# Kernel optimization log

Measured on AMD Instinct MI355X. Metric: run time of the kernel, lower is better.

## Reference

```python
import jax, jax.numpy as jnp
import numpy as np

N, T, D_FEAT, H = 8192, 60, 6, 64
NEG_SLOPE = 0.01  # torch LeakyReLU default


def setup_inputs() -> dict:
    key = jax.random.key(0)
    ks = jax.random.split(key, 20)
    s = lambda k, shape, fan: jax.random.normal(k, shape, jnp.float32) * (1.0 / np.sqrt(fan))
    inp = {
        'x': jax.random.normal(ks[0], (N, T, D_FEAT), jnp.float32),
        # LSTM layer 0 (input D_FEAT) and layer 1 (input H); gate order i,f,g,o
        'Wih0': s(ks[1], (4 * H, D_FEAT), H), 'Whh0': s(ks[2], (4 * H, H), H),
        'bih0': s(ks[3], (4 * H,), H), 'bhh0': s(ks[4], (4 * H,), H),
        'Wih1': s(ks[5], (4 * H, H), H), 'Whh1': s(ks[6], (4 * H, H), H),
        'bih1': s(ks[7], (4 * H,), H), 'bhh1': s(ks[8], (4 * H,), H),
        # GAT layer: transformation Linear(H,H) and attention vector a [2H,1] (randn in torch)
        'Wt': s(ks[9], (H, H), H), 'bt': s(ks[10], (H,), H),
        'a': jax.random.normal(ks[11], (2 * H, 1), jnp.float32),
        # fc and fc_out
        'Wfc': s(ks[12], (H, H), H), 'bfc': s(ks[13], (H,), H),
        'Wout': s(ks[14], (1, H), H), 'bout': s(ks[15], (1,), H),
    }
    return inp


def _lstm_layer(x, Wih, Whh, bih, bhh):
    # x: [N, T, Din] -> outputs [N, T, H]
    xg = jnp.einsum('ntd,gd->ntg', x, Wih) + bih + bhh  # precompute input gates

    def step(carry, xt):
        h, c = carry
        gates = xt + h @ Whh.T  # [N, 4H]
        i, f, g, o = jnp.split(gates, 4, axis=-1)
        c = jax.nn.sigmoid(f) * c + jax.nn.sigmoid(i) * jnp.tanh(g)
        h = jax.nn.sigmoid(o) * jnp.tanh(c)
        return (h, c), h

    n = x.shape[0]
    h0 = jnp.zeros((n, Whh.shape[1]), x.dtype)
    (_, _), hs = jax.lax.scan(step, (h0, h0), jnp.swapaxes(xg, 0, 1))
    return jnp.swapaxes(hs, 0, 1)


def _gat_layer(x, Wt, bt, a):
    # att[i,j] = leaky_relu(a1 . Wx_j + a2 . Wx_i); softmax over j; out = att @ x
    h = x @ Wt.T + bt                    # [N, H]
    hdim = h.shape[1]
    s1 = (h @ a[:hdim]).squeeze(-1)      # a1 . Wx_j  -> column term
    s2 = (h @ a[hdim:]).squeeze(-1)      # a2 . Wx_i  -> row term
    scores = jax.nn.leaky_relu(s2[:, None] + s1[None, :], NEG_SLOPE)  # [N, N]
    att = jax.nn.softmax(scores, axis=1)
    return att @ x


def reference(x, Wih0, Whh0, bih0, bhh0, Wih1, Whh1, bih1, bhh1,
              Wt, bt, a, Wfc, bfc, Wout, bout):
    out = _lstm_layer(x, Wih0, Whh0, bih0, bhh0)
    out = _lstm_layer(out, Wih1, Whh1, bih1, bhh1)
    last = out[:, -1, :]                 # [N, H]
    hidden = _gat_layer(last, Wt, bt, a) + last  # num_layers_gat = 1
    hidden = jax.nn.leaky_relu(hidden @ Wfc.T + bfc, NEG_SLOPE)
    return (hidden @ Wout.T + bout).squeeze(-1)  # [N]
```

## Files before the change

### kernel.cpp

```cpp
#include <hip/hip_runtime.h>

#define NN 8192
#define TT 60
#define DF 6
#define HH 64
#define GG 256
#define RS 132
#define CH 32
#define NB 256

typedef _Float16 half8 __attribute__((ext_vector_type(8)));
typedef float f32x4 __attribute__((ext_vector_type(4)));
#define MFMA16(a, b, c) __builtin_amdgcn_mfma_f32_16x16x32_f16((a), (b), (c), 0, 0, 0)

#define LOG2E 1.44269504f

__device__ __forceinline__ float lrelu_(float x) { return x > 0.0f ? x : 0.01f * x; }

__device__ __forceinline__ float lstm_act2s(float gi, float gf, float gg, float go,
                                            float& c)
{
    const float ei = __builtin_amdgcn_exp2f(gi);
    const float ef = __builtin_amdgcn_exp2f(gf);
    const float eg = __builtin_amdgcn_exp2f(fminf(gg, 63.f));
    const float sf = __builtin_amdgcn_rcpf(1.f + ef);
    const float tg_si = (1.f - eg) * __builtin_amdgcn_rcpf((1.f + ei) * (1.f + eg));
    c = __builtin_fmaf(sf, c, tg_si);
    const float eo = __builtin_amdgcn_exp2f(go);
    const float ec = __builtin_amdgcn_exp2f(fminf(c * (-2.f * LOG2E), 63.f));
    return (1.f - ec) * __builtin_amdgcn_rcpf((1.f + eo) * (1.f + ec));
}

__device__ __forceinline__ half8 ldw8s(const float* __restrict__ p, float s) {
    const float4* q = (const float4*)p;
    float4 u = q[0], v = q[1];
    half8 r;
    r[0]=(_Float16)(u.x*s); r[1]=(_Float16)(u.y*s); r[2]=(_Float16)(u.z*s); r[3]=(_Float16)(u.w*s);
    r[4]=(_Float16)(v.x*s); r[5]=(_Float16)(v.y*s); r[6]=(_Float16)(v.z*s); r[7]=(_Float16)(v.w*s);
    return r;
}

#define SXW (TT * 8 + 8)

__global__ __launch_bounds__(512, 4)
void lstm_fused_kernel(const float* __restrict__ x,
                       const float* __restrict__ Wih0, const float* __restrict__ Whh0,
                       const float* __restrict__ bih0, const float* __restrict__ bhh0,
                       const float* __restrict__ Wih1, const float* __restrict__ Whh1,
                       const float* __restrict__ bih1, const float* __restrict__ bhh1,
                       const float* __restrict__ Wt, const float* __restrict__ bt,
                       const float* __restrict__ av,
                       float* __restrict__ last_out,
                       float* __restrict__ s1g, float* __restrict__ s2g)
{
    __shared__ _Float16 sxp[16][SXW];
    __shared__ _Float16 h0buf[2][16][72];
    __shared__ _Float16 h1buf[2][16][72];
    __shared__ _Float16 zero16[8];
    __shared__ float sv1[HH], sv2[HH], sc12[2];

    const int tid  = threadIdx.x;
    const int w    = tid >> 6;
    const int grp  = w >> 2;
    const int cg   = w & 3;
    const int lane = tid & 63;
    const int quad = lane >> 4;
    const int l15  = lane & 15;
    const int hc   = cg * 16 + l15;
    const int n0   = blockIdx.x * 16;

    for (int i = tid; i < 16 * SXW / 2; i += 512) ((unsigned*)sxp)[i] = 0u;
    for (int i = tid; i < 2 * 16 * 72 / 2; i += 512) ((unsigned*)h0buf)[i] = 0u;
    for (int i = tid; i < 2 * 16 * 72 / 2; i += 512) ((unsigned*)h1buf)[i] = 0u;
    if (tid < 4) ((unsigned*)zero16)[tid] = 0u;
    __syncthreads();

    for (int idx = tid; idx < 16 * TT * DF; idx += 512) {
        const int m = idx / (TT * DF);
        const int r = idx - m * (TT * DF);
        const int t = r / DF;
        const int d = r - t * DF;
        sxp[m][t * 8 + d] = (_Float16)x[(size_t)(n0 + m) * (TT * DF) + r];
    }

    if (tid < HH) {
        float a1 = 0.f, a2 = 0.f;
        #pragma unroll 8
        for (int h = 0; h < HH; h++) {
            const float wt = Wt[h * HH + tid];
            a1 += wt * av[h];
            a2 += wt * av[HH + h];
        }
        sv1[tid] = a1; sv2[tid] = a2;
    } else if (tid == 64 || tid == 65) {
        const float* ap = av + (tid - 64) * HH;
        float c = 0.f;
        #pragma unroll 8
        for (int h = 0; h < HH; h++) c += bt[h] * ap[h];
        sc12[tid - 64] = c;
    }

    half8 wA[4][2], wB[4][2];
    float bias[4];
    half8 hzero;
    #pragma unroll
    for (int j = 0; j < 8; j++) hzero[j] = (_Float16)0.f;

    if (grp == 0) {
        #pragma unroll
        for (int nt = 0; nt < 4; nt++) {
            const float sc = (nt == 2) ? (-2.f * LOG2E) : (-LOG2E);
            const int g = nt * 64 + hc;
            wA[nt][0] = ldw8s(Whh0 + (size_t)g * HH + quad * 8, sc);
            wA[nt][1] = ldw8s(Whh0 + (size_t)g * HH + 32 + quad * 8, sc);
            bias[nt]  = (bih0[g] + bhh0[g]) * sc;
            half8 t = hzero;
            if (quad == 0) {
                #pragma unroll
                for (int j = 0; j < DF; j++) t[j] = (_Float16)(Wih0[g * DF + j] * sc);
            }
            wB[nt][0] = t;
            wB[nt][1] = hzero;
        }
    } else {
        #pragma unroll
        for (int nt = 0; nt < 4; nt++) {
            const float sc = (nt == 2) ? (-2.f * LOG2E) : (-LOG2E);
            const int g = nt * 64 + hc;
            wA[nt][0] = ldw8s(Wih1 + (size_t)g * HH + quad * 8, sc);
            wA[nt][1] = ldw8s(Wih1 + (size_t)g * HH + 32 + quad * 8, sc);
            wB[nt][0] = ldw8s(Whh1 + (size_t)g * HH + quad * 8, sc);
            wB[nt][1] = ldw8s(Whh1 + (size_t)g * HH + 32 + quad * 8, sc);
            bias[nt]  = (bih1[g] + bhh1[g]) * sc;
        }
    }

    float cs[4] = {0.f, 0.f, 0.f, 0.f};
    __syncthreads();

    for (int i = 0; i <= TT; i++) {
        const int p = i & 1;
        if (grp == 0) {
            if (i < TT) {
                const half8 a0 = *(const half8*)&h0buf[p][l15][quad * 8];
                const half8 a1 = *(const half8*)&h0buf[p][l15][32 + quad * 8];
                const _Float16* xap = (quad == 0) ? &sxp[l15][i * 8] : zero16;
                const half8 ax = *(const half8*)xap;
                f32x4 gv[4];
                #pragma unroll
                for (int nt = 0; nt < 4; nt++) {
                    f32x4 c; c[0] = bias[nt]; c[1] = bias[nt]; c[2] = bias[nt]; c[3] = bias[nt];
                    c = MFMA16(ax, wB[nt][0], c);
                    c = MFMA16(a0, wA[nt][0], c);
                    c = MFMA16(a1, wA[nt][1], c);
                    gv[nt] = c;
                }
                _Float16 (*h0w)[72] = h0buf[p ^ 1];
                #pragma unroll
                for (int reg = 0; reg < 4; reg++) {
                    const float hv = lstm_act2s(gv[0][reg], gv[1][reg], gv[2][reg], gv[3][reg], cs[reg]);
                    h0w[quad * 4 + reg][hc] = (_Float16)hv;
                }
            }
        } else {
            if (i > 0) {
                const half8 a00 = *(const half8*)&h0buf[p][l15][quad * 8];
                const half8 a01 = *(const half8*)&h0buf[p][l15][32 + quad * 8];
                const half8 a10 = *(const half8*)&h1buf[p][l15][quad * 8];
                const half8 a11 = *(const half8*)&h1buf[p][l15][32 + quad * 8];
                f32x4 gv[4];
                #pragma unroll
                for (int nt = 0; nt < 4; nt++) {
                    f32x4 c; c[0] = bias[nt]; c[1] = bias[nt]; c[2] = bias[nt]; c[3] = bias[nt];
                    c = MFMA16(a00, wA[nt][0], c);
                    c = MFMA16(a01, wA[nt][1], c);
                    c = MFMA16(a10, wB[nt][0], c);
                    c = MFMA16(a11, wB[nt][1], c);
                    gv[nt] = c;
                }
                _Float16 (*h1w)[72] = h1buf[p ^ 1];
                #pragma unroll
                for (int reg = 0; reg < 4; reg++) {
                    const float hv = lstm_act2s(gv[0][reg], gv[1][reg], gv[2][reg], gv[3][reg], cs[reg]);
                    h1w[quad * 4 + reg][hc] = (_Float16)hv;
                    if (i == TT) last_out[(size_t)(n0 + quad * 4 + reg) * HH + hc] = hv;
                }
            }
        }
        __syncthreads();
    }

    {
        const _Float16 (*hf)[72] = h1buf[1];
        const int r  = tid >> 5;
        const int c0 = tid & 31;
        const float h1a = (float)hf[r][c0];
        const float h1b = (float)hf[r][c0 + 32];
        float p1 = h1a * sv1[c0] + h1b * sv1[c0 + 32];
        float p2 = h1a * sv2[c0] + h1b * sv2[c0 + 32];
        #pragma unroll
        for (int off = 16; off > 0; off >>= 1) {
            p1 += __shfl_xor(p1, off);
            p2 += __shfl_xor(p2, off);
        }
        if (c0 == 0) {
            s1g[n0 + r] = p1 + sc12[0];
            s2g[n0 + r] = p2 + sc12[1];
        }
    }
}

__global__ __launch_bounds__(1024)
void rankfac_kernel(const float* __restrict__ s1g, const float* __restrict__ s2g,
                    float* __restrict__ Z, float* __restrict__ Ai, float* __restrict__ Bi,
                    float* __restrict__ U, float* __restrict__ W,
                    int* __restrict__ iperm, float* __restrict__ sortedD)
{
    __shared__ float sb[NN];
    __shared__ float sredw[16];
    __shared__ int   sRank[32];
    const int tid  = threadIdx.x;
    const int lane = tid & 63;
    const int wv   = tid >> 6;
    const int b    = blockIdx.x;
    const int j0   = b * 32;

    {
        const float4* g4 = (const float4*)s1g;
        float4* s4 = (float4*)sb;
        for (int idx = tid; idx < NN / 4; idx += 1024) s4[idx] = g4[idx];
    }
    if (tid < 32) sRank[tid] = 0;
    __syncthreads();

    float m = -1e30f;
    for (int idx = tid; idx < NN; idx += 1024) m = fmaxf(m, sb[idx]);
    #pragma unroll
    for (int off = 32; off > 0; off >>= 1) m = fmaxf(m, __shfl_xor(m, off));
    if (lane == 0) sredw[wv] = m;
    __syncthreads();
    if (tid == 0) {
        float mm = sredw[0];
        #pragma unroll
        for (int q = 1; q < 16; q++) mm = fmaxf(mm, sredw[q]);
        sredw[0] = mm;
    }
    __syncthreads();
    const float s1max = sredw[0];

    if (tid < 32) {
        const int j = j0 + tid;
        const float z  = s2g[j] + s1max;
        const float mi = lrelu_(z);
        Z[j]  = z;
        Ai[j] = __expf(z - mi);
        Bi[j] = __expf(0.01f * z - mi);
        const float d = sb[j] - s1max;
        U[j] = __expf(d);
        W[j] = __expf(0.01f * d);
    }
    {
        const int jl = tid & 31;
        const int part = tid >> 5;
        const float sj = sb[j0 + jl];
        const int jg = j0 + jl;
        const int k0 = part * (NN / 32);
        const float4* sb4 = (const float4*)&sb[k0];
        int cnt = 0;
        #pragma unroll 8
        for (int it = 0; it < NN / 32 / 4; it++) {
            const float4 v = sb4[it];
            const int kb = k0 + it * 4;
            cnt += (v.x < sj || (v.x == sj && kb + 0 < jg)) ? 1 : 0;
            cnt += (v.y < sj || (v.y == sj && kb + 1 < jg)) ? 1 : 0;
            cnt += (v.z < sj || (v.z == sj && kb + 2 < jg)) ? 1 : 0;
            cnt += (v.w < sj || (v.w == sj && kb + 3 < jg)) ? 1 : 0;
        }
        atomicAdd(&sRank[jl], cnt);
    }
    __syncthreads();
    if (tid < 32) {
        const int r = sRank[tid];
        iperm[r] = j0 + tid;
        sortedD[r] = sb[j0 + tid] - s1max;
    }
}

__global__ __launch_bounds__(256)
void scanA_kernel(const float* __restrict__ last, const float* __restrict__ U,
                  const float* __restrict__ W, const int* __restrict__ iperm,
                  float* __restrict__ chunkSum)
{
    __shared__ int   sj[CH];
    __shared__ float su[CH], sw[CH];
    __shared__ float al[CH][HH], bl[CH][HH];
    const int tid = threadIdx.x;
    const int b   = blockIdx.x;
    if (tid < CH) {
        const int j = iperm[b * CH + tid];
        sj[tid] = j; su[tid] = U[j]; sw[tid] = W[j];
    }
    __syncthreads();
    for (int idx = tid; idx < CH * HH; idx += 256) {
        const int rr = idx >> 6, c = idx & 63;
        const float lv = last[(size_t)sj[rr] * HH + c];
        al[rr][c] = su[rr] * lv;
        bl[rr][c] = sw[rr] * lv;
    }
    __syncthreads();
    if (tid < 130) {
        const int c = tid;
        float s = 0.f;
        if (c < 64) {
            for (int rr = 0; rr < CH; rr++) s += al[rr][c];
        } else if (c < 128) {
            for (int rr = 0; rr < CH; rr++) s += bl[rr][c - 64];
        } else if (c == 128) {
            for (int rr = 0; rr < CH; rr++) s += su[rr];
        } else {
            for (int rr = 0; rr < CH; rr++) s += sw[rr];
        }
        chunkSum[b * RS + c] = s;
    }
}

__global__ __launch_bounds__(1024)
void scanC_kernel(const float* __restrict__ last, const float* __restrict__ U,
                  const float* __restrict__ W, const int* __restrict__ iperm,
                  const float* __restrict__ chunkSum, float* __restrict__ PP)
{
    __shared__ int   sj[CH];
    __shared__ float su[CH], sw[CH];
    __shared__ float al[CH][HH], bl[CH][HH];
    __shared__ float pref[130][4];
    const int tid = threadIdx.x;
    const int b   = blockIdx.x;
    if (tid < CH) {
        const int j = iperm[b * CH + tid];
        sj[tid] = j; su[tid] = U[j]; sw[tid] = W[j];
    }
    __syncthreads();
    for (int idx = tid; idx < CH * HH; idx += 1024) {
        const int rr = idx >> 6, c = idx & 63;
        const float lv = last[(size_t)sj[rr] * HH + c];
        al[rr][c] = su[rr] * lv;
        bl[rr][c] = sw[rr] * lv;
    }
    {
        const int c   = tid >> 2;
        const int seg = tid & 3;
        if (c < 130) {
            const bool rev = (c < 64) || (c == 128);
            const int k0 = seg * (NB / 4);
            float s = 0.f;
            #pragma unroll 8
            for (int k = k0; k < k0 + NB / 4; k++) {
                const bool take = rev ? (k > b) : (k < b);
                s += take ? chunkSum[k * RS + c] : 0.f;
            }
            pref[c][seg] = s;
        }
    }
    __syncthreads();
    if (tid < 130) {
        const int c = tid;
        const bool rev = (c < 64) || (c == 128);
        float run = (pref[c][0] + pref[c][1]) + (pref[c][2] + pref[c][3]);
        if (rev) {
            if (b == NB - 1) PP[(size_t)NN * RS + c] = 0.f;
            for (int rr = CH - 1; rr >= 0; rr--) {
                const float val = (c < 64) ? al[rr][c] : su[rr];
                run += val;
                PP[(size_t)(b * CH + rr) * RS + c] = run;
            }
        } else {
            for (int rr = 0; rr < CH; rr++) {
                PP[(size_t)(b * CH + rr) * RS + c] = run;
                run += (c < 128) ? bl[rr][c - 64] : sw[rr];
            }
            if (b == NB - 1) PP[(size_t)NN * RS + c] = run;
        }
    }
}

__global__ __launch_bounds__(256)
void applyfc_kernel(const float* __restrict__ last,
                    const float* __restrict__ Z, const float* __restrict__ Ai, const float* __restrict__ Bi,
                    const float* __restrict__ sortedD, const float* __restrict__ PP,
                    const float* __restrict__ Wfc, const float* __restrict__ bfc,
                    const float* __restrict__ Wout, const float* __restrict__ bout,
                    float* __restrict__ out)
{
    __shared__ float sdD[NN];
    __shared__ float sW[HH][HH + 1];
    __shared__ float sbF[HH], saF[HH];
    const int tid = threadIdx.x;
    {
        const float4* g4 = (const float4*)sortedD;
        float4* s4 = (float4*)sdD;
        for (int idx = tid; idx < NN / 4; idx += 256) s4[idx] = g4[idx];
    }
    for (int idx = tid; idx < HH * HH; idx += 256) {
        const int h = idx >> 6, d = idx & 63;
        sW[d][h] = Wfc[idx];
    }
    if (tid < HH) { sbF[tid] = bfc[tid]; saF[tid] = Wout[tid]; }
    __syncthreads();

    const int wv = tid >> 6, lane = tid & 63;
    const int i0 = blockIdx.x * 16 + wv * 4;
    float zi[4]; int lo[4], hi[4];
    #pragma unroll
    for (int q = 0; q < 4; q++) { zi[q] = Z[i0 + q]; lo[q] = 0; hi[q] = NN; }
    for (int iter = 0; iter < 13; iter++) {
        #pragma unroll
        for (int q = 0; q < 4; q++) {
            if (lo[q] < hi[q]) {
                const int mid = (lo[q] + hi[q]) >> 1;
                const float dm = sdD[mid];
                if (zi[q] + dm > 0.f) hi[q] = mid; else lo[q] = mid + 1;
            }
        }
    }
    float gv[4];
    #pragma unroll
    for (int q = 0; q < 4; q++) {
        const int i = i0 + q;
        const float* rowp = PP + (size_t)lo[q] * RS;
        const float pu  = rowp[lane];
        const float pw  = rowp[64 + lane];
        const float pud = rowp[128];
        const float pwd = rowp[129];
        const float ai = Ai[i], bi = Bi[i];
        const float numer = bi * pw + ai * pu;
        const float den   = bi * pwd + ai * pud;
        const float lv = last[(size_t)i * HH + lane];
        gv[q] = numer * __builtin_amdgcn_rcpf(den) + lv;
    }
    const float bo = bout[0];
    #pragma unroll
    for (int q = 0; q < 4; q++) {
        float acc = sbF[lane];
        #pragma unroll
        for (int d = 0; d < HH; d++) acc += __shfl(gv[q], d) * sW[d][lane];
        float prod = lrelu_(acc) * saF[lane];
        #pragma unroll
        for (int off = 32; off > 0; off >>= 1) prod += __shfl_xor(prod, off);
        if (lane == 0) out[i0 + q] = prod + bo;
    }
}

extern "C" void kernel_launch(void* const* d_in, const int* in_sizes, int n_in,
                              void* d_out, int out_size, void* d_ws, size_t ws_size,
                              hipStream_t stream)
{
    (void)in_sizes; (void)n_in; (void)out_size; (void)ws_size;
    const float* x    = (const float*)d_in[0];
    const float* Wih0 = (const float*)d_in[1];
    const float* Whh0 = (const float*)d_in[2];
    const float* bih0 = (const float*)d_in[3];
    const float* bhh0 = (const float*)d_in[4];
    const float* Wih1 = (const float*)d_in[5];
    const float* Whh1 = (const float*)d_in[6];
    const float* bih1 = (const float*)d_in[7];
    const float* bhh1 = (const float*)d_in[8];
    const float* Wt   = (const float*)d_in[9];
    const float* bt   = (const float*)d_in[10];
    const float* a    = (const float*)d_in[11];
    const float* Wfc  = (const float*)d_in[12];
    const float* bfc  = (const float*)d_in[13];
    const float* Wout = (const float*)d_in[14];
    const float* bout = (const float*)d_in[15];
    float* out = (float*)d_out;

    float* ws       = (float*)d_ws;
    float* last     = ws;
    float* s1g      = last + (size_t)NN*HH;
    float* s2g      = s1g + NN;
    float* Z        = s2g + NN;
    float* Ai       = Z + NN;
    float* Bi       = Ai + NN;
    float* U        = Bi + NN;
    float* W        = U + NN;
    float* sortedD  = W + NN;
    int*   iperm    = (int*)(sortedD + NN);
    float* chunkSum = (float*)(iperm + NN);
    float* chunkOfs = chunkSum + NB*RS;
    float* PP       = chunkOfs + NB*RS;

    lstm_fused_kernel<<<dim3(NN / 16), dim3(512), 0, stream>>>(
        x, Wih0, Whh0, bih0, bhh0, Wih1, Whh1, bih1, bhh1,
        Wt, bt, a, last, s1g, s2g);
    rankfac_kernel<<<dim3(NB), dim3(1024), 0, stream>>>(
        s1g, s2g, Z, Ai, Bi, U, W, iperm, sortedD);
    scanA_kernel<<<dim3(NB), dim3(256), 0, stream>>>(last, U, W, iperm, chunkSum);
    scanC_kernel<<<dim3(NB), dim3(1024), 0, stream>>>(last, U, W, iperm, chunkSum, PP);
    applyfc_kernel<<<dim3(NN / 16), dim3(256), 0, stream>>>(
        last, Z, Ai, Bi, sortedD, PP, Wfc, bfc, Wout, bout, out);
}
```

Measured before the change: 235.4 us.

## Fuse chunk-sum scan pass into rank kernel via atomic scatter

Removes the separate scanA kernel launch. The rank kernel now scatters each element's weighted last-row contributions into its sorted-chunk sums using global float atomics, and the LSTM kernel zeroes the chunk-sum buffer beforehand. This saves one launch and the gather pass through iperm. In exchange it adds atomic contention on the chunk sums and makes the float summation order nondeterministic.

After: 240.3 us. 1.02x slower.

```diff
diff --git a/kernel.cpp b/kernel.cpp
--- a/kernel.cpp
+++ b/kernel.cpp
@@ -51,7 +51,8 @@
                        const float* __restrict__ Wt, const float* __restrict__ bt,
                        const float* __restrict__ av,
                        float* __restrict__ last_out,
-                       float* __restrict__ s1g, float* __restrict__ s2g)
+                       float* __restrict__ s1g, float* __restrict__ s2g,
+                       float* __restrict__ chunkSumZ)
 {
     __shared__ _Float16 sxp[16][SXW];
     __shared__ _Float16 h0buf[2][16][72];
@@ -68,6 +69,11 @@
     const int l15  = lane & 15;
     const int hc   = cg * 16 + l15;
     const int n0   = blockIdx.x * 16;
+
+    {
+        const int gidx = blockIdx.x * 512 + tid;
+        if (gidx < NB * RS) chunkSumZ[gidx] = 0.f;
+    }
 
     for (int i = tid; i < 16 * SXW / 2; i += 512) ((unsigned*)sxp)[i] = 0u;
     for (int i = tid; i < 2 * 16 * 72 / 2; i += 512) ((unsigned*)h0buf)[i] = 0u;
@@ -212,13 +218,16 @@
 
 __global__ __launch_bounds__(1024)
 void rankfac_kernel(const float* __restrict__ s1g, const float* __restrict__ s2g,
+                    const float* __restrict__ last,
                     float* __restrict__ Z, float* __restrict__ Ai, float* __restrict__ Bi,
                     float* __restrict__ U, float* __restrict__ W,
-                    int* __restrict__ iperm, float* __restrict__ sortedD)
+                    int* __restrict__ iperm, float* __restrict__ sortedD,
+                    float* __restrict__ chunkSum)
 {
     __shared__ float sb[NN];
     __shared__ float sredw[16];
     __shared__ int   sRank[32];
+    __shared__ float sU2[32], sW2[32];
     const int tid  = threadIdx.x;
     const int lane = tid & 63;
     const int wv   = tid >> 6;
@@ -256,8 +265,10 @@
         Ai[j] = __expf(z - mi);
         Bi[j] = __expf(0.01f * z - mi);
         const float d = sb[j] - s1max;
-        U[j] = __expf(d);
-        W[j] = __expf(0.01f * d);
+        const float u = __expf(d);
+        const float w2 = __expf(0.01f * d);
+        U[j] = u;  W[j] = w2;
+        sU2[tid] = u;  sW2[tid] = w2;
     }
     {
         const int jl = tid & 31;
@@ -284,43 +295,21 @@
         iperm[r] = j0 + tid;
         sortedD[r] = sb[j0 + tid] - s1max;
     }
-}
-
-__global__ __launch_bounds__(256)
-void scanA_kernel(const float* __restrict__ last, const float* __restrict__ U,
-                  const float* __restrict__ W, const int* __restrict__ iperm,
-                  float* __restrict__ chunkSum)
-{
-    __shared__ int   sj[CH];
-    __shared__ float su[CH], sw[CH];
-    __shared__ float al[CH][HH], bl[CH][HH];
-    const int tid = threadIdx.x;
-    const int b   = blockIdx.x;
-    if (tid < CH) {
-        const int j = iperm[b * CH + tid];
-        sj[tid] = j; su[tid] = U[j]; sw[tid] = W[j];
-    }
-    __syncthreads();
-    for (int idx = tid; idx < CH * HH; idx += 256) {
-        const int rr = idx >> 6, c = idx & 63;
-        const float lv = last[(size_t)sj[rr] * HH + c];
-        al[rr][c] = su[rr] * lv;
-        bl[rr][c] = sw[rr] * lv;
-    }
-    __syncthreads();
-    if (tid < 130) {
-        const int c = tid;
-        float s = 0.f;
-        if (c < 64) {
-            for (int rr = 0; rr < CH; rr++) s += al[rr][c];
-        } else if (c < 128) {
-            for (int rr = 0; rr < CH; rr++) s += bl[rr][c - 64];
-        } else if (c == 128) {
-            for (int rr = 0; rr < CH; rr++) s += su[rr];
-        } else {
-            for (int rr = 0; rr < CH; rr++) s += sw[rr];
-        }
-        chunkSum[b * RS + c] = s;
+
+    {
+        const int t  = tid >> 5;
+        const int c2 = tid & 31;
+        const int j  = j0 + t;
+        const int ch = sRank[t] >> 5;
+        float* dst = chunkSum + ch * RS;
+        const float u = sU2[t], w2 = sW2[t];
+        const float lv0 = last[(size_t)j * HH + c2];
+        const float lv1 = last[(size_t)j * HH + c2 + 32];
+        atomicAdd(&dst[c2],            u * lv0);
+        atomicAdd(&dst[c2 + 32],       u * lv1);
+        atomicAdd(&dst[64 + c2],       w2 * lv0);
+        atomicAdd(&dst[64 + c2 + 32],  w2 * lv1);
+        if (c2 == 0) { atomicAdd(&dst[128], u); atomicAdd(&dst[129], w2); }
     }
 }
 
@@ -490,10 +479,9 @@
 
     lstm_fused_kernel<<<dim3(NN / 16), dim3(512), 0, stream>>>(
         x, Wih0, Whh0, bih0, bhh0, Wih1, Whh1, bih1, bhh1,
-        Wt, bt, a, last, s1g, s2g);
+        Wt, bt, a, last, s1g, s2g, chunkSum);
     rankfac_kernel<<<dim3(NB), dim3(1024), 0, stream>>>(
-        s1g, s2g, Z, Ai, Bi, U, W, iperm, sortedD);
-    scanA_kernel<<<dim3(NB), dim3(256), 0, stream>>>(last, U, W, iperm, chunkSum);
+        s1g, s2g, last, Z, Ai, Bi, U, W, iperm, sortedD, chunkSum);
     scanC_kernel<<<dim3(NB), dim3(1024), 0, stream>>>(last, U, W, iperm, chunkSum, PP);
     applyfc_kernel<<<dim3(NN / 16), dim3(256), 0, stream>>>(
         last, Z, Ai, Bi, sortedD, PP, Wfc, bfc, Wout, bout, out);
```
